# Kernel tuning notes

Measured on AMD Instinct MI355X. Metric: run time of the kernel, lower is better.

Reference implementation:

```python
import jax, jax.numpy as jnp
from jax import lax
import numpy as np

B = 2048
N = 10  # wires on q_device0
C64 = jnp.complex64

# fixed gate matrices (qubit ordering matches wire-list order)
S_ = jnp.array([[1, 0], [0, 1j]], C64)
T_ = jnp.array([[1, 0], [0, np.exp(1j * np.pi / 4)]], C64)
SX_ = 0.5 * jnp.array([[1 + 1j, 1 - 1j], [1 - 1j, 1 + 1j]], C64)
Y_ = jnp.array([[0, -1j], [1j, 0]], C64)
CNOT_ = jnp.array([[1, 0, 0, 0], [0, 1, 0, 0], [0, 0, 0, 1], [0, 0, 1, 0]], C64)
CZ_ = jnp.diag(jnp.array([1, 1, 1, -1], C64))
CY_ = jnp.array([[1, 0, 0, 0], [0, 1, 0, 0], [0, 0, 0, -1j], [0, 0, 1j, 0]], C64)
SWAP_ = jnp.array([[1, 0, 0, 0], [0, 0, 1, 0], [0, 1, 0, 0], [0, 0, 0, 1]], C64)
_cs = np.eye(8); _cs[[5, 6]] = _cs[[6, 5]]  # CSWAP: |101> <-> |110>
CSWAP_ = jnp.array(_cs, C64)
_tf = np.eye(8); _tf[[6, 7]] = _tf[[7, 6]]  # Toffoli: |110> <-> |111>
TOFF_ = jnp.array(_tf, C64)

# parametrized single-qubit gate builders; t scalar -> [2,2], t [B] -> [B,2,2]
def _rx(t):
    c = jnp.cos(t / 2).astype(C64)
    s = -1j * jnp.sin(t / 2).astype(C64)
    return jnp.stack([jnp.stack([c, s], -1), jnp.stack([s, c], -1)], -2)

def _ry(t):
    c = jnp.cos(t / 2).astype(C64)
    s = jnp.sin(t / 2).astype(C64)
    return jnp.stack([jnp.stack([c, -s], -1), jnp.stack([s, c], -1)], -2)

def _rz(t):
    a = jnp.exp(-0.5j * t.astype(C64))
    b = jnp.exp(0.5j * t.astype(C64))
    z = jnp.zeros_like(a)
    return jnp.stack([jnp.stack([a, z], -1), jnp.stack([z, b], -1)], -2)

def _phase(t):
    e = jnp.exp(1j * t.astype(C64))
    o = jnp.ones_like(e)
    z = jnp.zeros_like(e)
    return jnp.stack([jnp.stack([o, z], -1), jnp.stack([z, e], -1)], -2)

def _rot(phi, th, om):  # RZ(om) RY(th) RZ(phi), pennylane/torchquantum convention
    c = jnp.cos(th / 2).astype(C64)
    s = jnp.sin(th / 2).astype(C64)
    p = phi.astype(C64); w = om.astype(C64)
    m00 = jnp.exp(-0.5j * (p + w)) * c
    m01 = -jnp.exp(0.5j * (p - w)) * s
    m10 = jnp.exp(-0.5j * (p - w)) * s
    m11 = jnp.exp(0.5j * (p + w)) * c
    return jnp.stack([jnp.stack([m00, m01], -1), jnp.stack([m10, m11], -1)], -2)

def _apply1(psi, U, w):  # psi: [B]+(2,)*N, U: [2,2] or [B,2,2]
    s = jnp.moveaxis(psi, w + 1, 1)
    if U.ndim == 2:
        s = jnp.einsum('ij,bj...->bi...', U, s)
    else:
        s = jnp.einsum('bij,bj...->bi...', U, s)
    return jnp.moveaxis(s, 1, w + 1)

def _applyk(psi, U, wires):  # fixed k-qubit gate, U: [2^k, 2^k]
    k = len(wires)
    axes = tuple(w + 1 for w in wires)
    s = jnp.moveaxis(psi, axes, tuple(range(1, k + 1)))
    sh = s.shape
    s = s.reshape((sh[0], 2 ** k) + sh[k + 1:])
    s = jnp.einsum('ij,bj...->bi...', U, s)
    return jnp.moveaxis(s.reshape(sh), tuple(range(1, k + 1)), axes)

def _forward(x, conv1_w, conv1_b, conv2_w, conv2_b, fc1_w, fc1_b, fc2_w, fc2_b,
             theta0, theta_rz, theta_ps, rot_p):
    dn = ('NCHW', 'OIHW', 'NCHW')
    h = lax.conv_general_dilated(x, conv1_w, (1, 1), 'VALID', dimension_numbers=dn)
    h = jax.nn.relu(h + conv1_b[None, :, None, None])
    h = lax.conv_general_dilated(h, conv2_w, (1, 1), 'VALID', dimension_numbers=dn)
    h = jax.nn.relu(h + conv2_b[None, :, None, None])
    h = lax.reduce_window(h, -jnp.inf, lax.max, (1, 1, 2, 2), (1, 1, 2, 2), 'VALID')
    h = h.reshape(h.shape[0], -1)  # [B, 9216], dropout = identity (eval)
    h = jax.nn.relu(h @ fc1_w.T + fc1_b)
    a = jax.nn.sigmoid(h @ fc2_w.T + fc2_b) * (2.0 * np.pi)  # angles [B, 10]
    bsz = a.shape[0]
    psi = jnp.zeros((bsz, 2 ** N), C64).at[:, 0].set(1.0).reshape((bsz,) + (2,) * N)
    trz = jnp.reshape(theta_rz, ())
    tps = jnp.reshape(theta_ps, ())
    for k in range(N):                      # TrainableRxAll
        psi = _apply1(psi, _rx(theta0[k]), k)
    for k in range(N):                      # RxAll with input angles
        psi = _apply1(psi, _rx(a[:, k]), k)
    psi = _apply1(psi, _rx(a[:, 1]), 1)
    psi = _apply1(psi, _rx(jnp.asarray(-np.pi / 4, jnp.float32)), 5)  # q_layer2 fixed
    psi = _apply1(psi, _ry(a[:, 2]), 2)
    psi = _apply1(psi, _rz(a[:, 3]), 3)
    psi = _apply1(psi, S_, 4)
    psi = _apply1(psi, T_, 5)
    psi = _apply1(psi, _rz(trz), 6)         # q_layer3
    psi = _apply1(psi, SX_, 7)
    # (q_device1 ops on a separate 3-wire device do not affect the output)
    psi = _applyk(psi, CZ_, (0, 5))
    psi = _applyk(psi, CNOT_, (0, 5))
    psi = _applyk(psi, CY_, (0, 5))
    psi = _applyk(psi, CY_, (3, 8))         # q_layer4
    psi = _applyk(psi, SWAP_, (2, 3))
    psi = _applyk(psi, CSWAP_, (4, 5, 6))
    psi = _applyk(psi, TOFF_, (8, 5, 0))    # q_layer5
    psi = _apply1(psi, _phase(tps), 8)      # q_layer6
    psi = _apply1(psi, _phase(a[:, 7]), 7)
    psi = _apply1(psi, _rot(rot_p[0], rot_p[1], rot_p[2]), 4)  # q_layer7
    psi = _apply1(psi, _rot(a[:, 6], a[:, 7], a[:, 8]), 5)
    axes = tuple(range(1, N + 1))
    evs = [jnp.real(jnp.sum(jnp.conj(psi) * _apply1(psi, Y_, k), axis=axes))
           for k in range(N)]
    ev = jnp.stack(evs, -1)                 # [B, 10] <Y_k>
    return jax.nn.log_softmax(ev, axis=1)


def setup_inputs() -> dict:
    key = jax.random.key(0)
    ks = jax.random.split(key, 13)
    return {
        'x': jax.random.normal(ks[0], (B, 1, 28, 28), jnp.float32),
        'conv1_w': jax.random.normal(ks[1], (32, 1, 3, 3), jnp.float32) * 0.2,
        'conv1_b': jnp.zeros((32,), jnp.float32),
        'conv2_w': jax.random.normal(ks[2], (64, 32, 3, 3), jnp.float32) * 0.05,
        'conv2_b': jnp.zeros((64,), jnp.float32),
        'fc1_w': jax.random.normal(ks[3], (128, 9216), jnp.float32) * 0.01,
        'fc1_b': jnp.zeros((128,), jnp.float32),
        'fc2_w': jax.random.normal(ks[4], (10, 128), jnp.float32) * 0.1,
        'fc2_b': jnp.zeros((10,), jnp.float32),
        'theta0': jax.random.normal(ks[5], (10,), jnp.float32),
        'theta_rz': jax.random.normal(ks[6], (1,), jnp.float32),
        'theta_ps': jax.random.normal(ks[7], (1,), jnp.float32),
        'rot_p': jax.random.normal(ks[8], (3,), jnp.float32),
    }


def reference(x, conv1_w, conv1_b, conv2_w, conv2_b, fc1_w, fc1_b, fc2_w, fc2_b,
              theta0, theta_rz, theta_ps, rot_p):
    return _forward(x, conv1_w, conv1_b, conv2_w, conv2_b, fc1_w, fc1_b, fc2_w, fc2_b,
                    theta0, theta_rz, theta_ps, rot_p)
```

## Files before the change

kernel.cpp:

```cpp
#include <hip/hip_runtime.h>
#include <math.h>

typedef short short8 __attribute__((ext_vector_type(8)));
typedef float f32x4 __attribute__((ext_vector_type(4)));
typedef float f32x16 __attribute__((ext_vector_type(16)));

#define GLB_CP(p) ((const __attribute__((address_space(1))) void*)(p))
#define LDS_CP(p) ((__attribute__((address_space(3))) void*)(p))

__device__ __forceinline__ float2 cmul(float2 a, float2 b) {
    return make_float2(a.x * b.x - a.y * b.y, a.x * b.y + a.y * b.x);
}

__device__ __forceinline__ ushort f2bf(float f) {
    uint u = __float_as_uint(f);
    uint r = (u + 0x7FFFu + ((u >> 16) & 1u)) >> 16;
    return (ushort)r;
}

__global__ __launch_bounds__(256) void conv1_prep_kernel(
    const float* __restrict__ x, const float* __restrict__ w1,
    const float* __restrict__ b1, ushort* __restrict__ h1b,
    const float* __restrict__ c2w, const float* __restrict__ f1w,
    ushort* __restrict__ wt2, ushort* __restrict__ wf1)
{
    __shared__ float wl[288];
    __shared__ float bl[32];
    int blk = blockIdx.x;
    int tid = threadIdx.x;
    if (blk >= 21632) {
        int i = (blk - 21632) * 256 + tid;
        if (i < 18432) {
            int icl = i & 7;
            int t = i >> 3;
            int oc = t & 63;
            int t2 = t >> 6;
            int icg = t2 & 3;
            int tap = t2 >> 2;
            int ic = icg * 8 + icl;
            wt2[i] = f2bf(c2w[(oc * 32 + ic) * 9 + tap]);
        } else if (i < 18432 + 1179648) {
            int j = i - 18432;
            wf1[j] = f2bf(f1w[j]);
        }
        return;
    }
    for (int e = tid; e < 288; e += 256) wl[e] = w1[e];
    if (tid < 32) bl[tid] = b1[tid];
    __syncthreads();
    int e = blk * 256 + tid;
    int icg = e & 3;
    int t = e >> 2;
    int pix = t % 676;
    int b = t / 676;
    int y = pix / 26, xc = pix % 26;
    const float* xp = x + b * 784 + y * 28 + xc;
    float in9[9];
#pragma unroll
    for (int ky = 0; ky < 3; ++ky)
#pragma unroll
        for (int kx = 0; kx < 3; ++kx) in9[ky * 3 + kx] = xp[ky * 28 + kx];
    short8 outv;
#pragma unroll
    for (int o = 0; o < 8; ++o) {
        int oc = icg * 8 + o;
        float acc = bl[oc];
#pragma unroll
        for (int k = 0; k < 9; ++k) acc = fmaf(in9[k], wl[oc * 9 + k], acc);
        outv[o] = (short)f2bf(fmaxf(acc, 0.f));
    }
    *(short8*)&h1b[((b * 4 + icg) * 676 + pix) * 8] = outv;
}

#define EPILOG(ACC0, ACC1, RX, RY)                                                         \
    {                                                                                      \
        int pcolb = (RX) * 4 + 2 * hi;                                                     \
        _Pragma("unroll")                                                                  \
        for (int q = 0; q < 2; ++q) {                                                      \
            int prow = (RY) * 2 + q;                                                       \
            int bs = 8 * q;                                                                \
            float m00 = fmaxf(fmaxf(ACC0[bs], ACC0[bs + 1]), fmaxf(ACC0[bs + 4], ACC0[bs + 5])); \
            float m01 = fmaxf(fmaxf(ACC0[bs + 2], ACC0[bs + 3]), fmaxf(ACC0[bs + 6], ACC0[bs + 7])); \
            uint pk0 = (uint)f2bf(fmaxf(m00 + bias0, 0.f)) | ((uint)f2bf(fmaxf(m01 + bias0, 0.f)) << 16); \
            *(uint*)&pout[lo * 144 + prow * 12 + pcolb] = pk0;                             \
            float m10 = fmaxf(fmaxf(ACC1[bs], ACC1[bs + 1]), fmaxf(ACC1[bs + 4], ACC1[bs + 5])); \
            float m11 = fmaxf(fmaxf(ACC1[bs + 2], ACC1[bs + 3]), fmaxf(ACC1[bs + 6], ACC1[bs + 7])); \
            uint pk1 = (uint)f2bf(fmaxf(m10 + bias1, 0.f)) | ((uint)f2bf(fmaxf(m11 + bias1, 0.f)) << 16); \
            *(uint*)&pout[(lo + 32) * 144 + prow * 12 + pcolb] = pk1;                      \
        }                                                                                  \
    }

__global__ __launch_bounds__(384, 2) void conv2_persist(
    const ushort* __restrict__ h1b, const ushort* __restrict__ wt2,
    const float* __restrict__ c2b, ushort* __restrict__ pooled)
{
    __shared__ __attribute__((aligned(16))) ushort wt_lds[18432];
    __shared__ __attribute__((aligned(16))) ushort in_lds[2][22016];
    int cu = blockIdx.x;
    int tid = threadIdx.x;
    int wave = tid >> 6;
    int lane = tid & 63;
    int lo = lane & 31;
    int hi = lane >> 5;

    for (int c = wave; c < 36; c += 6) {
        const ushort* src = wt2 + (size_t)(c * 64 + lane) * 8;
        __builtin_amdgcn_global_load_lds(GLB_CP(src), LDS_CP(wt_lds + c * 512), 16, 0, 0);
    }
    {
        const ushort* base = h1b + (size_t)(cu * 8) * 21632;
        for (int c = wave; c < 43; c += 6) {
            int e = c * 64 + lane;
            if (e > 2703) e = 2703;
            __builtin_amdgcn_global_load_lds(GLB_CP(base + (size_t)e * 8),
                                             LDS_CP(in_lds[0] + c * 512), 16, 0, 0);
        }
    }
    float bias0 = c2b[lo];
    float bias1 = c2b[lo + 32];
    __syncthreads();

    short8 A0r[9][2];
#pragma unroll
    for (int tap = 0; tap < 9; ++tap)
#pragma unroll
        for (int ks = 0; ks < 2; ++ks)
            A0r[tap][ks] = *(const short8*)&wt_lds[((tap * 4 + ks * 2 + hi) * 64 + lo) * 8];

    int pb[3];
#pragma unroll
    for (int i = 0; i < 3; ++i) {
        int r = wave + 6 * i;
        int rx = r % 3, ry = r / 3;
        int xcoord = rx * 8 + (lo & 7);
        int ycoord = ry * 4 + (lo >> 3);
        pb[i] = ycoord * 26 + xcoord;
    }
    int rx0 = wave % 3, ry0 = wave / 3;
    int rx1 = (wave + 6) % 3, ry1 = (wave + 6) / 3;
    int rx2 = (wave + 12) % 3, ry2 = (wave + 12) / 3;

    for (int j = 0; j < 8; ++j) {
        if (j < 7) {
            const ushort* base = h1b + (size_t)(cu * 8 + j + 1) * 21632;
            ushort* dst = in_lds[(j + 1) & 1];
            for (int c = wave; c < 43; c += 6) {
                int e = c * 64 + lane;
                if (e > 2703) e = 2703;
                __builtin_amdgcn_global_load_lds(GLB_CP(base + (size_t)e * 8),
                                                 LDS_CP(dst + c * 512), 16, 0, 0);
            }
        }

        const ushort* ib = in_lds[j & 1];
        f32x16 aA0 = (f32x16)0.f, aA1 = (f32x16)0.f;
        f32x16 aB0 = (f32x16)0.f, aB1 = (f32x16)0.f;
        f32x16 aC0 = (f32x16)0.f, aC1 = (f32x16)0.f;

#pragma unroll
        for (int tap = 0; tap < 9; ++tap) {
            int off = (tap / 3) * 26 + (tap % 3);
#pragma unroll
            for (int ks = 0; ks < 2; ++ks) {
                short8 a0 = A0r[tap][ks];
                short8 a1 = *(const short8*)&wt_lds[((tap * 4 + ks * 2 + hi) * 64 + 32 + lo) * 8];
                const ushort* ip = &ib[((ks * 2 + hi) * 676 + off) * 8];
                short8 b0 = *(const short8*)(ip + pb[0] * 8);
                short8 b1 = *(const short8*)(ip + pb[1] * 8);
                short8 b2 = *(const short8*)(ip + pb[2] * 8);
                aA0 = __builtin_amdgcn_mfma_f32_32x32x16_bf16(b0, a0, aA0, 0, 0, 0);
                aA1 = __builtin_amdgcn_mfma_f32_32x32x16_bf16(b0, a1, aA1, 0, 0, 0);
                aB0 = __builtin_amdgcn_mfma_f32_32x32x16_bf16(b1, a0, aB0, 0, 0, 0);
                aB1 = __builtin_amdgcn_mfma_f32_32x32x16_bf16(b1, a1, aB1, 0, 0, 0);
                aC0 = __builtin_amdgcn_mfma_f32_32x32x16_bf16(b2, a0, aC0, 0, 0, 0);
                aC1 = __builtin_amdgcn_mfma_f32_32x32x16_bf16(b2, a1, aC1, 0, 0, 0);
            }
        }

        ushort* pout = pooled + (size_t)(cu * 8 + j) * 9216;
        EPILOG(aA0, aA1, rx0, ry0)
        EPILOG(aB0, aB1, rx1, ry1)
        EPILOG(aC0, aC1, rx2, ry2)
        __syncthreads();
    }
}

__global__ __launch_bounds__(256) void fc1_mfma(
    const ushort* __restrict__ pooled, const ushort* __restrict__ wf1,
    float* __restrict__ part)
{
    int bx = blockIdx.x, by = blockIdx.y;
    int tid = threadIdx.x;
    int wid = tid >> 6, lane = tid & 63;
    int lo = lane & 15, hi = lane >> 4;
    int m0 = bx * 32;
    int kb = by * 2304;

    f32x4 acc[2][2];
#pragma unroll
    for (int mt = 0; mt < 2; ++mt)
#pragma unroll
        for (int j = 0; j < 2; ++j) acc[mt][j] = (f32x4)0.f;

    const ushort* arow0 = pooled + (size_t)(m0 + lo) * 9216 + kb + hi * 8;
    const ushort* arow1 = arow0 + 16 * 9216;
    const ushort* brow0 = wf1 + (size_t)(wid * 32 + lo) * 9216 + kb + hi * 8;
    const ushort* brow1 = brow0 + 16 * 9216;

    for (int kt = 0; kt < 72; ++kt) {
        short8 a0 = *(const short8*)(arow0 + kt * 32);
        short8 a1 = *(const short8*)(arow1 + kt * 32);
        short8 b0 = *(const short8*)(brow0 + kt * 32);
        short8 b1 = *(const short8*)(brow1 + kt * 32);
        acc[0][0] = __builtin_amdgcn_mfma_f32_16x16x32_bf16(a0, b0, acc[0][0], 0, 0, 0);
        acc[1][0] = __builtin_amdgcn_mfma_f32_16x16x32_bf16(a1, b0, acc[1][0], 0, 0, 0);
        acc[0][1] = __builtin_amdgcn_mfma_f32_16x16x32_bf16(a0, b1, acc[0][1], 0, 0, 0);
        acc[1][1] = __builtin_amdgcn_mfma_f32_16x16x32_bf16(a1, b1, acc[1][1], 0, 0, 0);
    }
    float* pp = part + (size_t)by * 262144;
#pragma unroll
    for (int mt = 0; mt < 2; ++mt)
#pragma unroll
        for (int j = 0; j < 2; ++j)
#pragma unroll
            for (int r = 0; r < 4; ++r)
                pp[(m0 + mt * 16 + hi * 4 + r) * 128 + wid * 32 + j * 16 + lo] = acc[mt][j][r];
}

__device__ __forceinline__ void apply_rot2(float2* s, int p, float2 m00, float2 m01,
                                           float2 m10, float2 m11, int tid)
{
    for (int q = tid; q < 512; q += 256) {
        int i0 = ((q >> p) << (p + 1)) | (q & ((1 << p) - 1));
        int i1 = i0 | (1 << p);
        float2 aa = s[i0], bb = s[i1];
        s[i0] = make_float2(m00.x * aa.x - m00.y * aa.y + m01.x * bb.x - m01.y * bb.y,
                            m00.x * aa.y + m00.y * aa.x + m01.x * bb.y + m01.y * bb.x);
        s[i1] = make_float2(m10.x * aa.x - m10.y * aa.y + m11.x * bb.x - m11.y * bb.y,
                            m10.x * aa.y + m10.y * aa.x + m11.x * bb.y + m11.y * bb.x);
    }
}

__global__ __launch_bounds__(256) void quantum_kernel(
    const float* __restrict__ part, const float* __restrict__ f1b,
    const float* __restrict__ f2w, const float* __restrict__ f2b,
    const float* __restrict__ theta0, const float* __restrict__ theta_rz,
    const float* __restrict__ theta_ps, const float* __restrict__ rot_p,
    float* __restrict__ out)
{
    __shared__ float2 s[1024];
    __shared__ float red[40];
    __shared__ float P[64];
    __shared__ float h[128];
    __shared__ float angs[16];
    int b = blockIdx.x;
    int tid = threadIdx.x;

    if (tid < 128) {
        float v = part[0 * 262144 + b * 128 + tid] + part[1 * 262144 + b * 128 + tid]
                + part[2 * 262144 + b * 128 + tid] + part[3 * 262144 + b * 128 + tid];
        h[tid] = fmaxf(v + f1b[tid], 0.f);
    }
    __syncthreads();
    if (tid < 10) {
        const float* wp = f2w + tid * 128;
        float sacc = f2b[tid];
        for (int k = 0; k < 128; ++k) sacc = fmaf(h[k], wp[k], sacc);
        angs[tid] = 6.28318530718f / (1.f + expf(-sacc));
    }
    __syncthreads();

    if (tid < 13) {
        if (tid < 10) {
            int k = tid;
            float ak = angs[k];
            float th = theta0[k] + ak;
            if (k == 1) th += ak;
            if (k == 5) th -= 0.78539816339745f;
            float c, sn; sincosf(0.5f * th, &sn, &c);
            float2 v0 = make_float2(c, 0.f), v1 = make_float2(0.f, -sn);
            if (k == 0) v1 = make_float2(-sn, 0.f);
            if (k == 2) { float ca, sa; sincosf(0.5f * ak, &sa, &ca);
                float2 n0 = make_float2(ca * v0.x - sa * v1.x, ca * v0.y - sa * v1.y);
                float2 n1 = make_float2(sa * v0.x + ca * v1.x, sa * v0.y + ca * v1.y);
                v0 = n0; v1 = n1; }
            if (k == 3) { float ca, sa; sincosf(0.5f * ak, &sa, &ca);
                v0 = cmul(v0, make_float2(ca, -sa));
                v1 = cmul(v1, make_float2(ca, sa)); }
            if (k == 4) { float2 t = v1; v1 = make_float2(-t.y, t.x); }
            if (k == 5) { const float r = 0.70710678118655f;
                float2 t = v1; v1 = make_float2(r * (t.x - t.y), r * (t.x + t.y)); }
            if (k == 6) { float ca, sa; sincosf(0.5f * theta_rz[0], &sa, &ca);
                v0 = cmul(v0, make_float2(ca, -sa));
                v1 = cmul(v1, make_float2(ca, sa)); }
            if (k == 7) { float2 p = v0, q = v1;
                v0 = make_float2(0.5f * ((p.x - p.y) + (q.x + q.y)),
                                 0.5f * ((p.x + p.y) + (q.y - q.x)));
                v1 = make_float2(0.5f * ((p.x + p.y) + (q.x - q.y)),
                                 0.5f * ((p.y - p.x) + (q.x + q.y)));
                float c2, s2; sincosf(ak, &s2, &c2);
                v1 = cmul(v1, make_float2(c2, s2)); }
            P[k * 4 + 0] = v0.x; P[k * 4 + 1] = v0.y;
            P[k * 4 + 2] = v1.x; P[k * 4 + 3] = v1.y;
        } else if (tid == 10) {
            float c1, s1; sincosf(theta_ps[0], &s1, &c1);
            P[40] = c1; P[41] = s1;
        } else if (tid == 11) {
            float c, sn; sincosf(0.5f * rot_p[1], &sn, &c);
            float A = 0.5f * (rot_p[0] + rot_p[2]), Bv = 0.5f * (rot_p[0] - rot_p[2]);
            float cA, sA; sincosf(A, &sA, &cA);
            float cB, sB; sincosf(Bv, &sB, &cB);
            P[44] = cA * c;  P[45] = -sA * c;
            P[46] = -cB * sn; P[47] = -sB * sn;
            P[48] = cB * sn;  P[49] = -sB * sn;
            P[50] = cA * c;  P[51] = sA * c;
        } else {
            float a6 = angs[6], a7 = angs[7], a8 = angs[8];
            float c, sn; sincosf(0.5f * a7, &sn, &c);
            float A = 0.5f * (a6 + a8), Bv = 0.5f * (a6 - a8);
            float cA, sA; sincosf(A, &sA, &cA);
            float cB, sB; sincosf(Bv, &sB, &cB);
            P[52] = cA * c;  P[53] = -sA * c;
            P[54] = -cB * sn; P[55] = -sB * sn;
            P[56] = cB * sn;  P[57] = -sB * sn;
            P[58] = cA * c;  P[59] = sA * c;
        }
    }
    __syncthreads();

    float2 v[10][2];
#pragma unroll
    for (int k = 0; k < 10; ++k) {
        int slot = (k == 2) ? 3 : (k == 3) ? 2 : k;
        v[k][0] = make_float2(P[slot * 4], P[slot * 4 + 1]);
        v[k][1] = make_float2(P[slot * 4 + 2], P[slot * 4 + 3]);
    }

    for (int i = tid; i < 1024; i += 256) {
        float2 c = ((i >> 9) & 1) ? v[0][1] : v[0][0];
#pragma unroll
        for (int k = 1; k < 10; ++k) {
            float2 vk = ((i >> (9 - k)) & 1) ? v[k][1] : v[k][0];
            c = cmul(c, vk);
        }
        s[i] = c;
    }
    __syncthreads();

    {
        int j = tid;
        float2 p1 = make_float2(P[40], P[41]);
        int i0 = (j & 1) | (((j >> 1) & 31) << 2) | (((j >> 6) & 3) << 8) | 128;
        int i1 = i0 | 2;
        float2 t0 = s[i0], t1 = s[i1];
        s[i0] = make_float2(t1.y, -t1.x);
        s[i1] = cmul(make_float2(-t0.y, t0.x), p1);
        int i2 = (j & 1) | 2 | (((j >> 1) & 31) << 2) | (((j >> 6) & 3) << 8);
        s[i2] = cmul(s[i2], p1);
    }
    __syncthreads();
    if (tid < 128) {
        int j = tid;
        int i0 = (j & 7) | 16 | 32 | (((j >> 3) & 15) << 6);
        int i1 = i0 ^ 0x18;
        float2 t0 = s[i0], t1 = s[i1];
        s[i0] = t1; s[i1] = t0;
    }
    __syncthreads();
    if (tid < 128) {
        int j = tid;
        int i0 = (j & 1) | 2 | (((j >> 1) & 3) << 2) | 16 | (((j >> 3) & 15) << 5);
        int i1 = i0 | 512;
        float2 t0 = s[i0], t1 = s[i1];
        s[i0] = t1; s[i1] = t0;
    }
    __syncthreads();
    apply_rot2(s, 5, make_float2(P[44], P[45]), make_float2(P[46], P[47]),
               make_float2(P[48], P[49]), make_float2(P[50], P[51]), tid);
    __syncthreads();
    apply_rot2(s, 4, make_float2(P[52], P[53]), make_float2(P[54], P[55]),
               make_float2(P[56], P[57]), make_float2(P[58], P[59]), tid);
    __syncthreads();

    int wave = tid >> 6;
    for (int k = 0; k < 10; ++k) {
        int p = 9 - k;
        float part_ = 0.f;
        for (int q = tid; q < 512; q += 256) {
            int i0 = ((q >> p) << (p + 1)) | (q & ((1 << p) - 1));
            int i1 = i0 | (1 << p);
            float2 aa = s[i0], bb = s[i1];
            part_ += aa.x * bb.y - aa.y * bb.x;
        }
        part_ *= 2.f;
#pragma unroll
        for (int off = 32; off > 0; off >>= 1)
            part_ += __shfl_down(part_, off, 64);
        if ((tid & 63) == 0) red[k * 4 + wave] = part_;
    }
    __syncthreads();
    if (tid == 0) {
        float ev[10];
        float mx = -1e30f;
#pragma unroll
        for (int k = 0; k < 10; ++k) {
            ev[k] = red[k * 4] + red[k * 4 + 1] + red[k * 4 + 2] + red[k * 4 + 3];
            mx = fmaxf(mx, ev[k]);
        }
        float sum = 0.f;
#pragma unroll
        for (int k = 0; k < 10; ++k) sum += expf(ev[k] - mx);
        float lse = mx + logf(sum);
#pragma unroll
        for (int k = 0; k < 10; ++k) out[b * 10 + k] = ev[k] - lse;
    }
}

extern "C" void kernel_launch(void* const* d_in, const int* in_sizes, int n_in,
                              void* d_out, int out_size, void* d_ws, size_t ws_size,
                              hipStream_t stream)
{
    (void)in_sizes; (void)n_in; (void)out_size; (void)ws_size;
    const float* x    = (const float*)d_in[0];
    const float* c1w  = (const float*)d_in[1];
    const float* c1b  = (const float*)d_in[2];
    const float* c2w  = (const float*)d_in[3];
    const float* c2b  = (const float*)d_in[4];
    const float* f1w  = (const float*)d_in[5];
    const float* f1b  = (const float*)d_in[6];
    const float* f2w  = (const float*)d_in[7];
    const float* f2b  = (const float*)d_in[8];
    const float* th0  = (const float*)d_in[9];
    const float* trz  = (const float*)d_in[10];
    const float* tps  = (const float*)d_in[11];
    const float* rotp = (const float*)d_in[12];
    float* out = (float*)d_out;

    char* ws = (char*)d_ws;
    ushort* h1b    = (ushort*)(ws);
    ushort* pooled = (ushort*)(ws + 88604672);
    ushort* wt2    = (ushort*)(ws + 126353408);
    ushort* wf1    = (ushort*)(ws + 126390272);
    float*  part   = (float*)(ws + 128749568);

    conv1_prep_kernel<<<26312, 256, 0, stream>>>(x, c1w, c1b, h1b, c2w, f1w, wt2, wf1);
    conv2_persist<<<256, 384, 0, stream>>>(h1b, wt2, c2b, pooled);
    fc1_mfma<<<dim3(64, 4), 256, 0, stream>>>(pooled, wf1, part);
    quantum_kernel<<<2048, 256, 0, stream>>>(part, f1b, f2w, f2b, th0, trz, tps, rotp, out);
}
```

Measured before the change: 140.5 us.

## Fuse conv1 into persistent conv2 kernel with producer waves computing next image

Removes the separate conv1 pass that wrote an ~88MB bf16 activation buffer to global memory and reread it in conv2. Each persistent block now loads raw 28x28 images into LDS, and two extra producer waves compute conv1 for the next image into the double-buffered input while six waves run the MFMA conv2 on the current one. The weight prep is split into its own small kernel. It trades HBM traffic for conv1 compute done by only 128 threads per block at 512 threads and one block per CU, which could leave the producer waves as the bottleneck. It also drops the register-cached A fragments in favour of LDS reads.

```diff
diff --git a/kernel.cpp b/kernel.cpp
--- a/kernel.cpp
+++ b/kernel.cpp
@@ -18,58 +18,51 @@
     return (ushort)r;
 }
 
-__global__ __launch_bounds__(256) void conv1_prep_kernel(
-    const float* __restrict__ x, const float* __restrict__ w1,
-    const float* __restrict__ b1, ushort* __restrict__ h1b,
+__global__ __launch_bounds__(256) void prep_kernel(
     const float* __restrict__ c2w, const float* __restrict__ f1w,
     ushort* __restrict__ wt2, ushort* __restrict__ wf1)
 {
-    __shared__ float wl[288];
-    __shared__ float bl[32];
-    int blk = blockIdx.x;
-    int tid = threadIdx.x;
-    if (blk >= 21632) {
-        int i = (blk - 21632) * 256 + tid;
-        if (i < 18432) {
-            int icl = i & 7;
-            int t = i >> 3;
-            int oc = t & 63;
-            int t2 = t >> 6;
-            int icg = t2 & 3;
-            int tap = t2 >> 2;
-            int ic = icg * 8 + icl;
-            wt2[i] = f2bf(c2w[(oc * 32 + ic) * 9 + tap]);
-        } else if (i < 18432 + 1179648) {
-            int j = i - 18432;
-            wf1[j] = f2bf(f1w[j]);
-        }
-        return;
-    }
-    for (int e = tid; e < 288; e += 256) wl[e] = w1[e];
-    if (tid < 32) bl[tid] = b1[tid];
-    __syncthreads();
-    int e = blk * 256 + tid;
-    int icg = e & 3;
-    int t = e >> 2;
-    int pix = t % 676;
-    int b = t / 676;
-    int y = pix / 26, xc = pix % 26;
-    const float* xp = x + b * 784 + y * 28 + xc;
-    float in9[9];
-#pragma unroll
-    for (int ky = 0; ky < 3; ++ky)
-#pragma unroll
-        for (int kx = 0; kx < 3; ++kx) in9[ky * 3 + kx] = xp[ky * 28 + kx];
-    short8 outv;
-#pragma unroll
-    for (int o = 0; o < 8; ++o) {
-        int oc = icg * 8 + o;
-        float acc = bl[oc];
-#pragma unroll
-        for (int k = 0; k < 9; ++k) acc = fmaf(in9[k], wl[oc * 9 + k], acc);
-        outv[o] = (short)f2bf(fmaxf(acc, 0.f));
-    }
-    *(short8*)&h1b[((b * 4 + icg) * 676 + pix) * 8] = outv;
+    int i = blockIdx.x * 256 + threadIdx.x;
+    if (i < 18432) {
+        int icl = i & 7;
+        int t = i >> 3;
+        int oc = t & 63;
+        int t2 = t >> 6;
+        int icg = t2 & 3;
+        int tap = t2 >> 2;
+        int ic = icg * 8 + icl;
+        wt2[i] = f2bf(c2w[(oc * 32 + ic) * 9 + tap]);
+    } else if (i < 18432 + 1179648) {
+        int j = i - 18432;
+        wf1[j] = f2bf(f1w[j]);
+    }
+}
+
+__device__ __forceinline__ void conv1_image(
+    const float* xs, const float* w1s, const float* b1s,
+    ushort* in_buf, int tstart, int tstride)
+{
+    for (int task = tstart; task < 2704; task += tstride) {
+        int icg = task & 3;
+        int pix = task >> 2;
+        int y = pix / 26, xc = pix % 26;
+        float in9[9];
+#pragma unroll
+        for (int ky = 0; ky < 3; ++ky)
+#pragma unroll
+            for (int kx = 0; kx < 3; ++kx)
+                in9[ky * 3 + kx] = xs[(y + ky) * 28 + xc + kx];
+        short8 ov;
+#pragma unroll
+        for (int o = 0; o < 8; ++o) {
+            int oc = icg * 8 + o;
+            float acc = b1s[oc];
+#pragma unroll
+            for (int k = 0; k < 9; ++k) acc = fmaf(in9[k], w1s[oc * 9 + k], acc);
+            ov[o] = (short)f2bf(fmaxf(acc, 0.f));
+        }
+        *(short8*)&in_buf[(icg * 676 + pix) * 8] = ov;
+    }
 }
 
 #define EPILOG(ACC0, ACC1, RX, RY)                                                         \
@@ -90,97 +83,100 @@
         }                                                                                  \
     }
 
-__global__ __launch_bounds__(384, 2) void conv2_persist(
-    const ushort* __restrict__ h1b, const ushort* __restrict__ wt2,
+__global__ __launch_bounds__(512, 1) void conv2_fused(
+    const float* __restrict__ x, const float* __restrict__ c1w,
+    const float* __restrict__ c1b, const ushort* __restrict__ wt2,
     const float* __restrict__ c2b, ushort* __restrict__ pooled)
 {
     __shared__ __attribute__((aligned(16))) ushort wt_lds[18432];
     __shared__ __attribute__((aligned(16))) ushort in_lds[2][22016];
+    __shared__ __attribute__((aligned(16))) float xs[2][1024];
+    __shared__ float w1s[288];
+    __shared__ float b1s[32];
     int cu = blockIdx.x;
     int tid = threadIdx.x;
-    int wave = tid >> 6;
+    int wid = tid >> 6;
     int lane = tid & 63;
     int lo = lane & 31;
     int hi = lane >> 5;
 
-    for (int c = wave; c < 36; c += 6) {
+    for (int c = wid; c < 36; c += 8) {
         const ushort* src = wt2 + (size_t)(c * 64 + lane) * 8;
         __builtin_amdgcn_global_load_lds(GLB_CP(src), LDS_CP(wt_lds + c * 512), 16, 0, 0);
     }
-    {
-        const ushort* base = h1b + (size_t)(cu * 8) * 21632;
-        for (int c = wave; c < 43; c += 6) {
+    for (int e = tid; e < 288; e += 512) w1s[e] = c1w[e];
+    if (tid < 32) b1s[tid] = c1b[tid];
+#pragma unroll
+    for (int img = 0; img < 2; ++img) {
+        const float* src = x + (size_t)(cu * 8 + img) * 784;
+        for (int c = wid; c < 4; c += 8) {
             int e = c * 64 + lane;
-            if (e > 2703) e = 2703;
-            __builtin_amdgcn_global_load_lds(GLB_CP(base + (size_t)e * 8),
-                                             LDS_CP(in_lds[0] + c * 512), 16, 0, 0);
+            if (e > 195) e = 195;
+            __builtin_amdgcn_global_load_lds(GLB_CP(src + e * 4),
+                                             LDS_CP(xs[img] + c * 256), 16, 0, 0);
         }
     }
     float bias0 = c2b[lo];
     float bias1 = c2b[lo + 32];
     __syncthreads();
 
-    short8 A0r[9][2];
-#pragma unroll
-    for (int tap = 0; tap < 9; ++tap)
-#pragma unroll
-        for (int ks = 0; ks < 2; ++ks)
-            A0r[tap][ks] = *(const short8*)&wt_lds[((tap * 4 + ks * 2 + hi) * 64 + lo) * 8];
+    conv1_image(xs[0], w1s, b1s, in_lds[0], tid, 512);
+    __syncthreads();
 
     int pb[3];
 #pragma unroll
     for (int i = 0; i < 3; ++i) {
-        int r = wave + 6 * i;
+        int r = wid + 6 * i;
         int rx = r % 3, ry = r / 3;
-        int xcoord = rx * 8 + (lo & 7);
-        int ycoord = ry * 4 + (lo >> 3);
-        pb[i] = ycoord * 26 + xcoord;
-    }
-    int rx0 = wave % 3, ry0 = wave / 3;
-    int rx1 = (wave + 6) % 3, ry1 = (wave + 6) / 3;
-    int rx2 = (wave + 12) % 3, ry2 = (wave + 12) / 3;
+        pb[i] = (ry * 4 + (lo >> 3)) * 26 + rx * 8 + (lo & 7);
+    }
+    int rx0 = wid % 3, ry0 = wid / 3;
+    int rx1 = (wid + 6) % 3, ry1 = (wid + 6) / 3;
+    int rx2 = (wid + 12) % 3, ry2 = (wid + 12) / 3;
 
     for (int j = 0; j < 8; ++j) {
-        if (j < 7) {
-            const ushort* base = h1b + (size_t)(cu * 8 + j + 1) * 21632;
-            ushort* dst = in_lds[(j + 1) & 1];
-            for (int c = wave; c < 43; c += 6) {
-                int e = c * 64 + lane;
-                if (e > 2703) e = 2703;
-                __builtin_amdgcn_global_load_lds(GLB_CP(base + (size_t)e * 8),
-                                                 LDS_CP(dst + c * 512), 16, 0, 0);
+        if (wid < 6) {
+            const ushort* ib = in_lds[j & 1];
+            f32x16 aA0 = (f32x16)0.f, aA1 = (f32x16)0.f;
+            f32x16 aB0 = (f32x16)0.f, aB1 = (f32x16)0.f;
+            f32x16 aC0 = (f32x16)0.f, aC1 = (f32x16)0.f;
+#pragma unroll
+            for (int tap = 0; tap < 9; ++tap) {
+                int off = (tap / 3) * 26 + (tap % 3);
+#pragma unroll
+                for (int ks = 0; ks < 2; ++ks) {
+                    const ushort* wp = &wt_lds[((tap * 4 + ks * 2 + hi) * 64) * 8];
+                    short8 a0 = *(const short8*)(wp + lo * 8);
+                    short8 a1 = *(const short8*)(wp + (32 + lo) * 8);
+                    const ushort* ip = &ib[((ks * 2 + hi) * 676 + off) * 8];
+                    short8 b0 = *(const short8*)(ip + pb[0] * 8);
+                    short8 b1 = *(const short8*)(ip + pb[1] * 8);
+                    short8 b2 = *(const short8*)(ip + pb[2] * 8);
+                    aA0 = __builtin_amdgcn_mfma_f32_32x32x16_bf16(b0, a0, aA0, 0, 0, 0);
+                    aA1 = __builtin_amdgcn_mfma_f32_32x32x16_bf16(b0, a1, aA1, 0, 0, 0);
+                    aB0 = __builtin_amdgcn_mfma_f32_32x32x16_bf16(b1, a0, aB0, 0, 0, 0);
+                    aB1 = __builtin_amdgcn_mfma_f32_32x32x16_bf16(b1, a1, aB1, 0, 0, 0);
+                    aC0 = __builtin_amdgcn_mfma_f32_32x32x16_bf16(b2, a0, aC0, 0, 0, 0);
+                    aC1 = __builtin_amdgcn_mfma_f32_32x32x16_bf16(b2, a1, aC1, 0, 0, 0);
+                }
             }
-        }
-
-        const ushort* ib = in_lds[j & 1];
-        f32x16 aA0 = (f32x16)0.f, aA1 = (f32x16)0.f;
-        f32x16 aB0 = (f32x16)0.f, aB1 = (f32x16)0.f;
-        f32x16 aC0 = (f32x16)0.f, aC1 = (f32x16)0.f;
-
-#pragma unroll
-        for (int tap = 0; tap < 9; ++tap) {
-            int off = (tap / 3) * 26 + (tap % 3);
-#pragma unroll
-            for (int ks = 0; ks < 2; ++ks) {
-                short8 a0 = A0r[tap][ks];
-                short8 a1 = *(const short8*)&wt_lds[((tap * 4 + ks * 2 + hi) * 64 + 32 + lo) * 8];
-                const ushort* ip = &ib[((ks * 2 + hi) * 676 + off) * 8];
-                short8 b0 = *(const short8*)(ip + pb[0] * 8);
-                short8 b1 = *(const short8*)(ip + pb[1] * 8);
-                short8 b2 = *(const short8*)(ip + pb[2] * 8);
-                aA0 = __builtin_amdgcn_mfma_f32_32x32x16_bf16(b0, a0, aA0, 0, 0, 0);
-                aA1 = __builtin_amdgcn_mfma_f32_32x32x16_bf16(b0, a1, aA1, 0, 0, 0);
-                aB0 = __builtin_amdgcn_mfma_f32_32x32x16_bf16(b1, a0, aB0, 0, 0, 0);
-                aB1 = __builtin_amdgcn_mfma_f32_32x32x16_bf16(b1, a1, aB1, 0, 0, 0);
-                aC0 = __builtin_amdgcn_mfma_f32_32x32x16_bf16(b2, a0, aC0, 0, 0, 0);
-                aC1 = __builtin_amdgcn_mfma_f32_32x32x16_bf16(b2, a1, aC1, 0, 0, 0);
+            ushort* pout = pooled + (size_t)(cu * 8 + j) * 9216;
+            EPILOG(aA0, aA1, rx0, ry0)
+            EPILOG(aB0, aB1, rx1, ry1)
+            EPILOG(aC0, aC1, rx2, ry2)
+        } else {
+            if (j + 2 <= 7) {
+                const float* src = x + (size_t)(cu * 8 + j + 2) * 784;
+                for (int c = (wid - 6) * 2; c < (wid - 6) * 2 + 2; ++c) {
+                    int e = c * 64 + lane;
+                    if (e > 195) e = 195;
+                    __builtin_amdgcn_global_load_lds(GLB_CP(src + e * 4),
+                                                     LDS_CP(xs[j & 1] + c * 256), 16, 0, 0);
+                }
             }
-        }
-
-        ushort* pout = pooled + (size_t)(cu * 8 + j) * 9216;
-        EPILOG(aA0, aA1, rx0, ry0)
-        EPILOG(aB0, aB1, rx1, ry1)
-        EPILOG(aC0, aC1, rx2, ry2)
+            if (j + 1 <= 7)
+                conv1_image(xs[(j + 1) & 1], w1s, b1s, in_lds[(j + 1) & 1], tid - 384, 128);
+        }
         __syncthreads();
     }
 }
@@ -437,14 +433,13 @@
     float* out = (float*)d_out;
 
     char* ws = (char*)d_ws;
-    ushort* h1b    = (ushort*)(ws);
-    ushort* pooled = (ushort*)(ws + 88604672);
-    ushort* wt2    = (ushort*)(ws + 126353408);
-    ushort* wf1    = (ushort*)(ws + 126390272);
-    float*  part   = (float*)(ws + 128749568);
-
-    conv1_prep_kernel<<<26312, 256, 0, stream>>>(x, c1w, c1b, h1b, c2w, f1w, wt2, wf1);
-    conv2_persist<<<256, 384, 0, stream>>>(h1b, wt2, c2b, pooled);
+    ushort* pooled = (ushort*)(ws);
+    ushort* wt2    = (ushort*)(ws + 37748736);
+    ushort* wf1    = (ushort*)(ws + 37785600);
+    float*  part   = (float*)(ws + 40144896);
+
+    prep_kernel<<<4680, 256, 0, stream>>>(c2w, f1w, wt2, wf1);
+    conv2_fused<<<256, 512, 0, stream>>>(x, c1w, c1b, wt2, c2b, pooled);
     fc1_mfma<<<dim3(64, 4), 256, 0, stream>>>(pooled, wf1, part);
     quantum_kernel<<<2048, 256, 0, stream>>>(part, f1b, f2w, f2b, th0, trz, tps, rotp, out);
 }
```

Result: faster. 135.0 us (-4.0%).
